# Kernel optimization log

Hardware: AMD Instinct MI355X
Metric: run time of the kernel (lower is better)

The kernel has to match this reference:

```python
import jax, jax.numpy as jnp
import numpy as np

T, B, D = 160, 640, 40      # time-major frames, batch (N_spk*M_utt), log-mel dim
H, P, L = 768, 256, 3       # nb_hidden, nb_proj, nb_layers


def setup_inputs() -> dict:
    key = jax.random.key(0)
    ks = jax.random.split(key, 1 + 3 * L)
    inp = {"x": jax.random.normal(ks[0], (T, B, D), jnp.float32)}
    din = D
    for l in range(L):
        gs = np.float32(np.sqrt(2.0 / (din + P + 4 * H)))  # glorot-ish scale
        inp[f"W{l}"] = jax.random.normal(ks[1 + 3 * l], (din + P, 4 * H), jnp.float32) * gs
        inp[f"b{l}"] = jnp.zeros((4 * H,), jnp.float32)
        ps = np.float32(np.sqrt(2.0 / (H + P)))
        inp[f"Wp{l}"] = jax.random.normal(ks[3 + 3 * l], (H, P), jnp.float32) * ps
        din = P
    return inp


def lstmp_layer(x, W, b, Wp):
    # x: [T, B, d_in] time-major. TF LSTMCell with num_proj: state h has dim P,
    # gate order (i, j, f, o), forget_bias = 1.0.
    bsz = x.shape[1]
    c0 = jnp.zeros((bsz, H), x.dtype)
    h0 = jnp.zeros((bsz, P), x.dtype)

    def step(carry, xt):
        c, h = carry
        z = jnp.concatenate([xt, h], axis=-1) @ W + b            # [B, 4H]
        i, j, f, o = jnp.split(z, 4, axis=-1)
        c = jax.nn.sigmoid(f + 1.0) * c + jax.nn.sigmoid(i) * jnp.tanh(j)
        h = (jax.nn.sigmoid(o) * jnp.tanh(c)) @ Wp               # projection -> [B, P]
        return (c, h), h

    _, ys = jax.lax.scan(step, (c0, h0), x)                      # ys: [T, B, P]
    return ys


def reference(x, W0, b0, Wp0, W1, b1, Wp1, W2, b2, Wp2):
    h = lstmp_layer(x, W0, b0, Wp0)
    h = lstmp_layer(h, W1, b1, Wp1)
    h = lstmp_layer(h, W2, b2, Wp2)
    emb = h[-1]                                                  # last timestep: [B, P]
    return emb / (jnp.linalg.norm(emb, axis=-1, keepdims=True) + 1e-6)
```

## Files before the change

### kernel.cpp

```cpp
#include <hip/hip_runtime.h>
#include <hip/hip_bf16.h>

typedef __attribute__((ext_vector_type(4))) float f32x4;
typedef __attribute__((ext_vector_type(8))) short s16x8;

#define DEVFN static __device__ __forceinline__

#define TT  160
#define BB  640
#define DD  40
#define HH  768
#define PP  256
#define G4H 3072

#define NWG   192
#define NTHR  512

#define KH  256
#define KX0 64

#define STW1 328
#define STW2 520
#define STP  776
#define LDS_ELEMS 66560

#define XP_BYTES   (TT*BB*64*2)
#define HR_BYTES   (3*4*BB*PP*2)
#define SB_BYTES   (3*4*BB*HH*2)
#define XP_OFF     0
#define HR_OFF     (XP_OFF + XP_BYTES)
#define SB_OFF     (HR_OFF + HR_BYTES)
#define SYNC_OFF   (SB_OFF + SB_BYTES)
#define SYNC_BYTES 4096

DEVFN float sigm(float v)  { return __fdividef(1.f, 1.f + __expf(-v)); }
DEVFN float tanh_(float v) { return 2.f * __fdividef(1.f, 1.f + __expf(-2.f * v)) - 1.f; }
DEVFN f32x4 f4zero() { f32x4 v; v[0]=0.f; v[1]=0.f; v[2]=0.f; v[3]=0.f; return v; }

DEVFN void gst_b16(__hip_bfloat16* p, __hip_bfloat16 v) {
  unsigned short u = __builtin_bit_cast(unsigned short, v);
  asm volatile("global_store_short %0, %1, off sc0 sc1" :: "v"(p), "v"(u));
}

DEVFN unsigned ld_cc(const unsigned* p) {
  unsigned v;
  asm volatile("global_load_dword %0, %1, off sc0 sc1\n\ts_waitcnt vmcnt(0)"
               : "=v"(v) : "v"(p) : "memory");
  return v;
}
DEVFN void st_cc(unsigned* p, unsigned v) {
  asm volatile("global_store_dword %0, %1, off sc0 sc1" :: "v"(p), "v"(v) : "memory");
}
DEVFN void ld3_cc(const unsigned* p0, const unsigned* p1, const unsigned* p2,
                  unsigned& a, unsigned& b, unsigned& c) {
  asm volatile("global_load_dword %0, %3, off sc0 sc1\n\t"
               "global_load_dword %1, %4, off sc0 sc1\n\t"
               "global_load_dword %2, %5, off sc0 sc1\n\t"
               "s_waitcnt vmcnt(0)"
               : "=&v"(a), "=&v"(b), "=&v"(c)
               : "v"(p0), "v"(p1), "v"(p2) : "memory");
}

DEVFN void fence_acq() { __builtin_amdgcn_fence(__ATOMIC_ACQUIRE, "agent"); }

#define SFLAG(s,l,g) ((s) + 256 + ((l)*48+(g))*4)
#define PFLAG(s,l,p) ((s) + 832 + ((l)*16+(p))*4)

DEVFN void init_barrier(unsigned* sync, int bid, int tid) {
  __syncthreads();
  if (tid == 0) st_cc(sync + bid, 1u);
  if (tid < 64) {
    unsigned a, b, c;
    for (;;) {
      ld3_cc(sync + tid, sync + 64 + tid, sync + 128 + tid, a, b, c);
      if (__all((a >= 1u) & (b >= 1u) & (c >= 1u))) break;
    }
    fence_acq();
  }
  __syncthreads();
}

DEVFN void wait_flags(const unsigned* base, int nf, int thr, int tid, bool dofence) {
  if (thr <= 0) return;
  if (tid < 64) {
    const unsigned* p = base + tid * 4;
    for (;;) {
      int v = (tid < nf) ? (int)ld_cc(p) : 0x7fffffff;
      if (__all(v >= thr)) break;
    }
    if (dofence) fence_acq();
  }
  __syncthreads();
}

DEVFN void wait_proj(const unsigned* sf_l, const unsigned* sf_lp1, int has2,
                     int thr1, int thr2, int tid, bool dofence) {
  if (tid < 64) {
    const unsigned* p1 = sf_l + tid * 4;
    const unsigned* p2 = sf_lp1 + tid * 4;
    for (;;) {
      int v1 = (tid < 24) ? (int)ld_cc(p1) : 0x7fffffff;
      int v2 = (has2 && tid < 24 && thr2 > 0) ? (int)ld_cc(p2) : 0x7fffffff;
      if (__all((v1 >= thr1) & (v2 >= thr2))) break;
    }
    if (dofence) fence_acq();
  }
  __syncthreads();
}

DEVFN void set_flag(unsigned* p, unsigned v, int tid) {
  __syncthreads();
  if (tid == 0) st_cc(p, v);
}

__global__ __launch_bounds__(NTHR, 1)
void lstmp_persistent(const float* __restrict__ xin,
                      const float* __restrict__ W0, const float* __restrict__ b0, const float* __restrict__ Wp0,
                      const float* __restrict__ W1, const float* __restrict__ b1, const float* __restrict__ Wp1,
                      const float* __restrict__ W2, const float* __restrict__ b2, const float* __restrict__ Wp2,
                      float* __restrict__ outp, unsigned char* __restrict__ ws)
{
  __shared__ __align__(16) __hip_bfloat16 lds[LDS_ELEMS];

  const int bid  = blockIdx.x;
  const int tid  = threadIdx.x;
  const int lane = tid & 63;
  const int wave = tid >> 6;
  const int q    = lane >> 4;
  const int c16  = lane & 15;

  __hip_bfloat16* Xp = (__hip_bfloat16*)(ws + XP_OFF);
  __hip_bfloat16* Hr = (__hip_bfloat16*)(ws + HR_OFF);
  __hip_bfloat16* Sb = (__hip_bfloat16*)(ws + SB_OFF);
  unsigned* sync     = (unsigned*)(ws + SYNC_OFF);

  const int xcd  = bid & 7;
  const int slot = bid >> 3;
  const bool isGate = (xcd < 6);
  int l = 0, bc = 0, hg = 0, mt = 0, nt = 0;
  if (isGate) { l = xcd >> 1; bc = xcd & 1; hg = slot; }
  else        { l = slot >> 3; int r = slot & 7; mt = (xcd - 6) * 2 + (r >> 2); nt = r & 3; }

  const int KX  = (l == 0) ? KX0 : 256;
  const int KT  = KX + KH;
  const int STW = (l == 0) ? STW1 : STW2;

  const float* Wl  = (l == 0) ? W0  : ((l == 1) ? W1  : W2);
  const float* bl  = (l == 0) ? b0  : ((l == 1) ? b1  : b2);
  const float* Wpl = (l == 0) ? Wp0 : ((l == 1) ? Wp1 : Wp2);

  for (int e = bid * NTHR + tid; e < TT * BB * 64; e += NWG * NTHR) {
    int k  = e & 63;
    int tb = e >> 6;
    float v = (k < DD) ? xin[(size_t)tb * DD + k] : 0.f;
    gst_b16(&Xp[e], __float2bfloat16(v));
  }

  if (isGate) {
    for (int idx = tid; idx < 128 * KT; idx += NTHR) {
      int kk = idx >> 7;
      int nn = idx & 127;
      int col = (nn >> 5) * HH + hg * 32 + (nn & 31);
      float v;
      if (l == 0) {
        v = (kk < DD) ? Wl[(size_t)kk * G4H + col]
                      : ((kk < KX0) ? 0.f : Wl[(size_t)(kk - 24) * G4H + col]);
      } else {
        v = Wl[(size_t)kk * G4H + col];
      }
      lds[nn * STW + kk] = __float2bfloat16(v);
    }
  } else {
    for (int idx = tid; idx < 64 * HH; idx += NTHR) {
      int kk = idx >> 6;
      int nn = idx & 63;
      lds[nn * STP + kk] = __float2bfloat16(Wpl[(size_t)kk * PP + nt * 64 + nn]);
    }
  }

  init_barrier(sync, bid, tid);

  if (isGate) {
    const int gid = bc * 24 + hg;
    unsigned* myflag = SFLAG(sync, l, gid);
    const unsigned* pf_own = PFLAG(sync, l, bc * 8);
    const unsigned* pf_prv = (l > 0) ? PFLAG(sync, l - 1, bc * 8) : PFLAG(sync, l, bc * 8);

    const int wmg = wave >> 1, wng = wave & 1;
    const int m0g = bc * 320 + wmg * 80;
    const int hcl = wng * 16 + c16;
    float biasv[4];
#pragma unroll
    for (int g = 0; g < 4; ++g) biasv[g] = bl[g * HH + hg * 32 + hcl];

    f32x4 acc[5][4];
    float cst[5][4];
#pragma unroll
    for (int mi = 0; mi < 5; ++mi)
#pragma unroll
      for (int g = 0; g < 4; ++g) { acc[mi][g] = f4zero(); cst[mi][g] = 0.f; }

    auto gate_gemm = [&](const __hip_bfloat16* A, int lda, int kbase, int klen) {
      s16x8 a0[5], a1[5];
#pragma unroll
      for (int mi = 0; mi < 5; ++mi)
        a0[mi] = *(const s16x8*)(A + (size_t)(m0g + mi * 16 + c16) * lda + 8 * q);
#pragma unroll 1
      for (int it2 = 0; it2 < klen / 64; ++it2) {
        const int ks0 = it2 * 64, ks1 = ks0 + 32;
#pragma unroll
        for (int mi = 0; mi < 5; ++mi)
          a1[mi] = *(const s16x8*)(A + (size_t)(m0g + mi * 16 + c16) * lda + ks1 + 8 * q);
        s16x8 bv[4];
#pragma unroll
        for (int g = 0; g < 4; ++g)
          bv[g] = *(const s16x8*)(lds + (g * 32 + hcl) * STW + kbase + ks0 + 8 * q);
#pragma unroll
        for (int mi = 0; mi < 5; ++mi)
#pragma unroll
          for (int g = 0; g < 4; ++g)
            acc[mi][g] = __builtin_amdgcn_mfma_f32_16x16x32_bf16(a0[mi], bv[g], acc[mi][g], 0, 0, 0);
        if (it2 + 1 < klen / 64) {
#pragma unroll
          for (int mi = 0; mi < 5; ++mi)
            a0[mi] = *(const s16x8*)(A + (size_t)(m0g + mi * 16 + c16) * lda + ks0 + 64 + 8 * q);
        }
#pragma unroll
        for (int g = 0; g < 4; ++g)
          bv[g] = *(const s16x8*)(lds + (g * 32 + hcl) * STW + kbase + ks1 + 8 * q);
#pragma unroll
        for (int mi = 0; mi < 5; ++mi)
#pragma unroll
          for (int g = 0; g < 4; ++g)
            acc[mi][g] = __builtin_amdgcn_mfma_f32_16x16x32_bf16(a1[mi], bv[g], acc[mi][g], 0, 0, 0);
      }
    };

    auto gate_update = [&](int t) {
      __hip_bfloat16* S = Sb + ((size_t)l * 4 + ((unsigned)t & 3)) * BB * HH;
#pragma unroll
      for (int mi = 0; mi < 5; ++mi) {
#pragma unroll
        for (int r = 0; r < 4; ++r) {
          float iv = acc[mi][0][r] + biasv[0];
          float jv = acc[mi][1][r] + biasv[1];
          float fv = acc[mi][2][r] + biasv[2];
          float ov = acc[mi][3][r] + biasv[3];
          float c  = sigm(fv + 1.f) * cst[mi][r] + sigm(iv) * tanh_(jv);
          cst[mi][r] = c;
          float sv = sigm(ov) * tanh_(c);
          gst_b16(&S[(size_t)(m0g + mi * 16 + q * 4 + r) * HH + hg * 32 + hcl],
                  __float2bfloat16(sv));
        }
#pragma unroll
        for (int g = 0; g < 4; ++g) acc[mi][g] = f4zero();
      }
    };

    if (l == 0) gate_gemm(Xp, 64, 0, KX0);
    else {
      wait_flags(pf_prv, 8, 1, tid, true);
      gate_gemm(Hr + ((size_t)(l - 1) * 4 + 1) * BB * PP, PP, 0, 256);
    }

    for (int t = 0; t < TT; ++t) {
      wait_flags(pf_own, 8, t, tid, (t & 3) == 0);
      gate_gemm(Hr + ((size_t)l * 4 + ((unsigned)t & 3)) * BB * PP, PP, KX, KH);
      gate_update(t);
      set_flag(myflag, (unsigned)(t + 1), tid);
      if (t + 1 < TT) {
        if (l == 0) gate_gemm(Xp + (size_t)(t + 1) * BB * 64, 64, 0, KX0);
        else {
          wait_flags(pf_prv, 8, t + 2, tid, false);
          gate_gemm(Hr + ((size_t)(l - 1) * 4 + ((unsigned)(t + 2) & 3)) * BB * PP, PP, 0, 256);
        }
      }
    }
  } else {
    const int pid = mt * 4 + nt;
    const int bch = mt >> 1;
    unsigned* myflag = PFLAG(sync, l, pid);
    const unsigned* sf_own = SFLAG(sync, l, bch * 24);
    const unsigned* sf_nxt = (l < 2) ? SFLAG(sync, l + 1, bch * 24) : SFLAG(sync, l, bch * 24);
    const int m0p = mt * 160 + ((wave & 3) >> 1) * 80;
    const int np0 = (wave & 1) * 32;

    for (int t = 0; t < TT; ++t) {
      wait_proj(sf_own, sf_nxt, l < 2 ? 1 : 0, t + 1, t - 3, tid, (t & 3) == 0);

      if (wave < 4) {
        const __hip_bfloat16* A = Sb + ((size_t)l * 4 + ((unsigned)t & 3)) * BB * HH;
        const __hip_bfloat16* ab[5];
#pragma unroll
        for (int mi = 0; mi < 5; ++mi)
          ab[mi] = A + (size_t)(m0p + mi * 16 + c16) * HH + 8 * q;

        f32x4 pa[5][2];
#pragma unroll
        for (int mi = 0; mi < 5; ++mi) { pa[mi][0] = f4zero(); pa[mi][1] = f4zero(); }

        s16x8 r0[5], r1[5], r2[5], r3[5];
#pragma unroll
        for (int mi = 0; mi < 5; ++mi) {
          r0[mi] = *(const s16x8*)(ab[mi] + 0);
          r1[mi] = *(const s16x8*)(ab[mi] + 32);
          r2[mi] = *(const s16x8*)(ab[mi] + 64);
          r3[mi] = *(const s16x8*)(ab[mi] + 96);
        }

#define PSLICE(RB, S)                                                          \
        {                                                                      \
          s16x8 bv0 = *(const s16x8*)(lds + (np0 + c16) * STP + (S) * 32 + 8 * q);      \
          s16x8 bv1 = *(const s16x8*)(lds + (np0 + 16 + c16) * STP + (S) * 32 + 8 * q); \
          _Pragma("unroll")                                                    \
          for (int mi = 0; mi < 5; ++mi) {                                     \
            pa[mi][0] = __builtin_amdgcn_mfma_f32_16x16x32_bf16(RB[mi], bv0, pa[mi][0], 0, 0, 0); \
            pa[mi][1] = __builtin_amdgcn_mfma_f32_16x16x32_bf16(RB[mi], bv1, pa[mi][1], 0, 0, 0); \
          }                                                                    \
          if ((S) + 4 < 24) {                                                  \
            _Pragma("unroll")                                                  \
            for (int mi = 0; mi < 5; ++mi)                                     \
              RB[mi] = *(const s16x8*)(ab[mi] + ((S) + 4) * 32);               \
          }                                                                    \
        }

        PSLICE(r0, 0)  PSLICE(r1, 1)  PSLICE(r2, 2)  PSLICE(r3, 3)
        PSLICE(r0, 4)  PSLICE(r1, 5)  PSLICE(r2, 6)  PSLICE(r3, 7)
        PSLICE(r0, 8)  PSLICE(r1, 9)  PSLICE(r2, 10) PSLICE(r3, 11)
        PSLICE(r0, 12) PSLICE(r1, 13) PSLICE(r2, 14) PSLICE(r3, 15)
        PSLICE(r0, 16) PSLICE(r1, 17) PSLICE(r2, 18) PSLICE(r3, 19)
        PSLICE(r0, 20) PSLICE(r1, 21) PSLICE(r2, 22) PSLICE(r3, 23)
#undef PSLICE

        __hip_bfloat16* Hd = Hr + ((size_t)l * 4 + ((unsigned)(t + 1) & 3)) * BB * PP;
#pragma unroll
        for (int mi = 0; mi < 5; ++mi)
#pragma unroll
          for (int ni = 0; ni < 2; ++ni)
#pragma unroll
            for (int r = 0; r < 4; ++r)
              gst_b16(&Hd[(size_t)(m0p + mi * 16 + q * 4 + r) * PP + nt * 64 + np0 + ni * 16 + c16],
                      __float2bfloat16(pa[mi][ni][r]));
      }

      set_flag(myflag, (unsigned)(t + 1), tid);
    }
  }

  wait_flags(PFLAG(sync, 2, 0), 16, TT, tid, true);
  const __hip_bfloat16* hf = Hr + (size_t)(2 * 4 + 0) * BB * PP;
  float* red = reinterpret_cast<float*>(lds);
  const int half = tid >> 8;
  const int col  = tid & 255;
  for (int row0 = bid * 2; row0 < BB; row0 += NWG * 2) {
    const int row = row0 + half;
    float v = __bfloat162float(hf[(size_t)row * PP + col]);
    float ssq = v * v;
#pragma unroll
    for (int off = 32; off > 0; off >>= 1) ssq += __shfl_down(ssq, off, 64);
    if (lane == 0) red[wave] = ssq;
    __syncthreads();
    float tot = red[half * 4 + 0] + red[half * 4 + 1] + red[half * 4 + 2] + red[half * 4 + 3];
    outp[(size_t)row * PP + col] = v * __fdividef(1.f, sqrtf(tot) + 1e-6f);
    __syncthreads();
  }
}

extern "C" void kernel_launch(void* const* d_in, const int* in_sizes, int n_in,
                              void* d_out, int out_size, void* d_ws, size_t ws_size,
                              hipStream_t stream) {
  (void)in_sizes; (void)n_in; (void)out_size; (void)ws_size;
  unsigned char* ws = (unsigned char*)d_ws;
  hipMemsetAsync(ws + HR_OFF, 0, HR_BYTES, stream);
  hipMemsetAsync(ws + SYNC_OFF, 0, SYNC_BYTES, stream);
  lstmp_persistent<<<dim3(NWG), dim3(NTHR), 0, stream>>>(
      (const float*)d_in[0],
      (const float*)d_in[1], (const float*)d_in[2], (const float*)d_in[3],
      (const float*)d_in[4], (const float*)d_in[5], (const float*)d_in[6],
      (const float*)d_in[7], (const float*)d_in[8], (const float*)d_in[9],
      (float*)d_out, ws);
}
```

Baseline: 5.335 ms.

## Fold projection into recurrent weights so gate blocks consume cell outputs directly

Precomputes Wp·W_h (768x3072 per layer) into LDS so each gate block multiplies the previous step's 768-wide cell output S instead of waiting for the projected h. This removes the gate-to-projection-to-gate dependency from the recurrent critical path, with each gate block now covering all 640 batch rows and 16 hidden units and waiting on all 48 gate flags. In exchange, recurrent K grows from 256 to 768 (three times the MFMA work per step), the bf16 rounding of the folded product differs from the reference, and setup does a 256-long scalar dot product per LDS weight element.

```diff
diff --git a/kernel.cpp b/kernel.cpp
--- a/kernel.cpp
+++ b/kernel.cpp
@@ -18,11 +18,12 @@
 
 #define KH  256
 #define KX0 64
-
-#define STW1 328
-#define STW2 520
+#define KS  768
+
+#define STW1 840
+#define STW2 1032
 #define STP  776
-#define LDS_ELEMS 66560
+#define LDS_ELEMS 66048
 
 #define XP_BYTES   (TT*BB*64*2)
 #define HR_BYTES   (3*4*BB*PP*2)
@@ -51,6 +52,12 @@
 DEVFN void st_cc(unsigned* p, unsigned v) {
   asm volatile("global_store_dword %0, %1, off sc0 sc1" :: "v"(p), "v"(v) : "memory");
 }
+DEVFN void ld2_cc(const unsigned* p0, const unsigned* p1, unsigned& a, unsigned& b) {
+  asm volatile("global_load_dword %0, %2, off sc0 sc1\n\t"
+               "global_load_dword %1, %3, off sc0 sc1\n\t"
+               "s_waitcnt vmcnt(0)"
+               : "=&v"(a), "=&v"(b) : "v"(p0), "v"(p1) : "memory");
+}
 DEVFN void ld3_cc(const unsigned* p0, const unsigned* p1, const unsigned* p2,
                   unsigned& a, unsigned& b, unsigned& c) {
   asm volatile("global_load_dword %0, %3, off sc0 sc1\n\t"
@@ -63,7 +70,7 @@
 
 DEVFN void fence_acq() { __builtin_amdgcn_fence(__ATOMIC_ACQUIRE, "agent"); }
 
-#define SFLAG(s,l,g) ((s) + 256 + ((l)*48+(g))*4)
+#define SFLAG(s,l,j) ((s) + 256 + ((l)*48+(j))*4)
 #define PFLAG(s,l,p) ((s) + 832 + ((l)*16+(p))*4)
 
 DEVFN void init_barrier(unsigned* sync, int bid, int tid) {
@@ -93,14 +100,33 @@
   __syncthreads();
 }
 
-DEVFN void wait_proj(const unsigned* sf_l, const unsigned* sf_lp1, int has2,
+DEVFN void gate_wait(const unsigned* sf, const unsigned* pfo, const unsigned* pfp,
+                     int hasprv, int t, int tid, bool dofence) {
+  if (tid < 64) {
+    const unsigned* p1 = (tid < 48) ? (sf + tid * 4) : (pfo + (tid - 48) * 4);
+    const int thr1     = (tid < 48) ? t : (t - 3);
+    const unsigned* p2 = (hasprv && tid >= 48) ? (pfp + (tid - 48) * 4) : p1;
+    const int thr2     = (hasprv && tid >= 48) ? (t + 1) : thr1;
+    for (;;) {
+      unsigned a, b;
+      ld2_cc(p1, p2, a, b);
+      if (__all(((int)a >= thr1) & ((int)b >= thr2))) break;
+    }
+    if (dofence) fence_acq();
+  }
+  __syncthreads();
+}
+
+DEVFN void proj_wait(const unsigned* s1, const unsigned* s2, int has2,
                      int thr1, int thr2, int tid, bool dofence) {
   if (tid < 64) {
-    const unsigned* p1 = sf_l + tid * 4;
-    const unsigned* p2 = sf_lp1 + tid * 4;
+    const unsigned* p1 = (tid < 48) ? (s1 + tid * 4) : s1;
+    const unsigned* p2 = (has2 && tid < 48) ? (s2 + tid * 4) : p1;
     for (;;) {
-      int v1 = (tid < 24) ? (int)ld_cc(p1) : 0x7fffffff;
-      int v2 = (has2 && tid < 24 && thr2 > 0) ? (int)ld_cc(p2) : 0x7fffffff;
+      unsigned a, b;
+      ld2_cc(p1, p2, a, b);
+      int v1 = (tid < 48) ? (int)a : 0x7fffffff;
+      int v2 = (has2 && tid < 48 && thr2 > 0) ? (int)b : 0x7fffffff;
       if (__all((v1 >= thr1) & (v2 >= thr2))) break;
     }
     if (dofence) fence_acq();
@@ -137,12 +163,11 @@
   const int xcd  = bid & 7;
   const int slot = bid >> 3;
   const bool isGate = (xcd < 6);
-  int l = 0, bc = 0, hg = 0, mt = 0, nt = 0;
-  if (isGate) { l = xcd >> 1; bc = xcd & 1; hg = slot; }
+  int l = 0, hg = 0, mt = 0, nt = 0;
+  if (isGate) { l = xcd >> 1; hg = (xcd & 1) * 24 + slot; }
   else        { l = slot >> 3; int r = slot & 7; mt = (xcd - 6) * 2 + (r >> 2); nt = r & 3; }
 
   const int KX  = (l == 0) ? KX0 : 256;
-  const int KT  = KX + KH;
   const int STW = (l == 0) ? STW1 : STW2;
 
   const float* Wl  = (l == 0) ? W0  : ((l == 1) ? W1  : W2);
@@ -157,18 +182,24 @@
   }
 
   if (isGate) {
-    for (int idx = tid; idx < 128 * KT; idx += NTHR) {
-      int kk = idx >> 7;
-      int nn = idx & 127;
-      int col = (nn >> 5) * HH + hg * 32 + (nn & 31);
-      float v;
-      if (l == 0) {
-        v = (kk < DD) ? Wl[(size_t)kk * G4H + col]
-                      : ((kk < KX0) ? 0.f : Wl[(size_t)(kk - 24) * G4H + col]);
-      } else {
-        v = Wl[(size_t)kk * G4H + col];
-      }
+    for (int idx = tid; idx < 64 * KX; idx += NTHR) {
+      int kk = idx >> 6;
+      int nn = idx & 63;
+      int col = (nn >> 4) * HH + hg * 16 + (nn & 15);
+      float v = (l == 0) ? ((kk < DD) ? Wl[(size_t)kk * G4H + col] : 0.f)
+                         : Wl[(size_t)kk * G4H + col];
       lds[nn * STW + kk] = __float2bfloat16(v);
+    }
+    const int din = (l == 0) ? DD : 256;
+    for (int idx = tid; idx < 64 * KS; idx += NTHR) {
+      int nn   = idx & 63;
+      int hrow = idx >> 6;
+      int col  = (nn >> 4) * HH + hg * 16 + (nn & 15);
+      float a0 = 0.f;
+#pragma unroll 4
+      for (int k = 0; k < PP; ++k)
+        a0 += Wpl[(size_t)hrow * PP + k] * Wl[(size_t)(din + k) * G4H + col];
+      lds[nn * STW + KX + hrow] = __float2bfloat16(a0);
     }
   } else {
     for (int idx = tid; idx < 64 * HH; idx += NTHR) {
@@ -181,17 +212,15 @@
   init_barrier(sync, bid, tid);
 
   if (isGate) {
-    const int gid = bc * 24 + hg;
-    unsigned* myflag = SFLAG(sync, l, gid);
-    const unsigned* pf_own = PFLAG(sync, l, bc * 8);
-    const unsigned* pf_prv = (l > 0) ? PFLAG(sync, l - 1, bc * 8) : PFLAG(sync, l, bc * 8);
-
-    const int wmg = wave >> 1, wng = wave & 1;
-    const int m0g = bc * 320 + wmg * 80;
-    const int hcl = wng * 16 + c16;
+    unsigned* myflag = SFLAG(sync, l, hg);
+    const unsigned* sf_own = SFLAG(sync, l, 0);
+    const unsigned* pf_own = PFLAG(sync, l, 0);
+    const unsigned* pf_prv = (l > 0) ? PFLAG(sync, l - 1, 0) : PFLAG(sync, l, 0);
+
+    const int m0g = wave * 80;
     float biasv[4];
 #pragma unroll
-    for (int g = 0; g < 4; ++g) biasv[g] = bl[g * HH + hg * 32 + hcl];
+    for (int g = 0; g < 4; ++g) biasv[g] = bl[g * HH + hg * 16 + c16];
 
     f32x4 acc[5][4];
     float cst[5][4];
@@ -214,7 +243,7 @@
         s16x8 bv[4];
 #pragma unroll
         for (int g = 0; g < 4; ++g)
-          bv[g] = *(const s16x8*)(lds + (g * 32 + hcl) * STW + kbase + ks0 + 8 * q);
+          bv[g] = *(const s16x8*)(lds + (g * 16 + c16) * STW + kbase + ks0 + 8 * q);
 #pragma unroll
         for (int mi = 0; mi < 5; ++mi)
 #pragma unroll
@@ -227,7 +256,7 @@
         }
 #pragma unroll
         for (int g = 0; g < 4; ++g)
-          bv[g] = *(const s16x8*)(lds + (g * 32 + hcl) * STW + kbase + ks1 + 8 * q);
+          bv[g] = *(const s16x8*)(lds + (g * 16 + c16) * STW + kbase + ks1 + 8 * q);
 #pragma unroll
         for (int mi = 0; mi < 5; ++mi)
 #pragma unroll
@@ -249,7 +278,7 @@
           float c  = sigm(fv + 1.f) * cst[mi][r] + sigm(iv) * tanh_(jv);
           cst[mi][r] = c;
           float sv = sigm(ov) * tanh_(c);
-          gst_b16(&S[(size_t)(m0g + mi * 16 + q * 4 + r) * HH + hg * 32 + hcl],
+          gst_b16(&S[(size_t)(m0g + mi * 16 + q * 4 + r) * HH + hg * 16 + c16],
                   __float2bfloat16(sv));
         }
 #pragma unroll
@@ -257,36 +286,23 @@
       }
     };
 
-    if (l == 0) gate_gemm(Xp, 64, 0, KX0);
-    else {
-      wait_flags(pf_prv, 8, 1, tid, true);
-      gate_gemm(Hr + ((size_t)(l - 1) * 4 + 1) * BB * PP, PP, 0, 256);
-    }
-
     for (int t = 0; t < TT; ++t) {
-      wait_flags(pf_own, 8, t, tid, (t & 3) == 0);
-      gate_gemm(Hr + ((size_t)l * 4 + ((unsigned)t & 3)) * BB * PP, PP, KX, KH);
+      gate_wait(sf_own, pf_own, pf_prv, l > 0, t, tid, (t & 3) == 0);
+      if (l == 0) gate_gemm(Xp + (size_t)t * BB * 64, 64, 0, KX0);
+      else        gate_gemm(Hr + ((size_t)(l - 1) * 4 + ((unsigned)(t + 1) & 3)) * BB * PP, PP, 0, 256);
+      if (t > 0) gate_gemm(Sb + ((size_t)l * 4 + ((unsigned)(t - 1) & 3)) * BB * HH, HH, KX, KS);
       gate_update(t);
       set_flag(myflag, (unsigned)(t + 1), tid);
-      if (t + 1 < TT) {
-        if (l == 0) gate_gemm(Xp + (size_t)(t + 1) * BB * 64, 64, 0, KX0);
-        else {
-          wait_flags(pf_prv, 8, t + 2, tid, false);
-          gate_gemm(Hr + ((size_t)(l - 1) * 4 + ((unsigned)(t + 2) & 3)) * BB * PP, PP, 0, 256);
-        }
-      }
     }
   } else {
-    const int pid = mt * 4 + nt;
-    const int bch = mt >> 1;
-    unsigned* myflag = PFLAG(sync, l, pid);
-    const unsigned* sf_own = SFLAG(sync, l, bch * 24);
-    const unsigned* sf_nxt = (l < 2) ? SFLAG(sync, l + 1, bch * 24) : SFLAG(sync, l, bch * 24);
+    unsigned* myflag = PFLAG(sync, l, mt * 4 + nt);
+    const unsigned* sf_own = SFLAG(sync, l, 0);
+    const unsigned* sf_nxt = (l < 2) ? SFLAG(sync, l + 1, 0) : SFLAG(sync, l, 0);
     const int m0p = mt * 160 + ((wave & 3) >> 1) * 80;
     const int np0 = (wave & 1) * 32;
 
     for (int t = 0; t < TT; ++t) {
-      wait_proj(sf_own, sf_nxt, l < 2 ? 1 : 0, t + 1, t - 3, tid, (t & 3) == 0);
+      proj_wait(sf_own, sf_nxt, l < 2 ? 1 : 0, t + 1, t - 3, tid, (t & 3) == 0);
 
       if (wave < 4) {
         const __hip_bfloat16* A = Sb + ((size_t)l * 4 + ((unsigned)t & 3)) * BB * HH;
```

New measurement: 8.012 ms. +50.2%, slower.
